# Performance work log

Measured on AMD Instinct MI355X. Metric: run time of the kernel, lower is better.

Reference implementation:

```python
import jax, jax.numpy as jnp
import numpy as np

N = 50000
E = 1600000
IN_C = 165
HID = 256
HEADS = 8
OUT_C = 2
NEG_SLOPE = 0.2


def setup_inputs() -> dict:
    key = jax.random.key(0)
    ks = jax.random.split(key, 10)
    x = jax.random.normal(ks[0], (N, IN_C), dtype=jnp.float32)
    edge_index = jax.random.randint(ks[1], (2, E), 0, N, dtype=jnp.int64)
    c1 = HID // HEADS  # 32 per-head channels in layer 1
    W1 = jax.random.normal(ks[2], (IN_C, HEADS * c1), dtype=jnp.float32) * (1.0 / np.sqrt(IN_C))
    att_src1 = jax.random.normal(ks[3], (HEADS, c1), dtype=jnp.float32) * 0.1
    att_dst1 = jax.random.normal(ks[4], (HEADS, c1), dtype=jnp.float32) * 0.1
    b1 = jnp.zeros((HEADS * c1,), dtype=jnp.float32)
    W2 = jax.random.normal(ks[5], (HID, 1 * OUT_C), dtype=jnp.float32) * (1.0 / np.sqrt(HID))
    att_src2 = jax.random.normal(ks[6], (1, OUT_C), dtype=jnp.float32) * 0.1
    att_dst2 = jax.random.normal(ks[7], (1, OUT_C), dtype=jnp.float32) * 0.1
    b2 = jnp.zeros((OUT_C,), dtype=jnp.float32)
    return {"x": x, "edge_index": edge_index, "W1": W1, "att_src1": att_src1,
            "att_dst1": att_dst1, "b1": b1, "W2": W2, "att_src2": att_src2,
            "att_dst2": att_dst2, "b2": b2}


def _gat_conv(x, src, dst, W, att_src, att_dst, bias, heads, concat):
    """PyG GATConv (eval mode, self-loops already appended to src/dst)."""
    n = x.shape[0]
    c = att_src.shape[1]
    h = (x @ W).reshape(n, heads, c)                      # [N, H, C]
    a_src = jnp.einsum('nhc,hc->nh', h, att_src)          # [N, H]
    a_dst = jnp.einsum('nhc,hc->nh', h, att_dst)
    e = a_src[src] + a_dst[dst]                           # [Et, H]
    e = jax.nn.leaky_relu(e, NEG_SLOPE)
    # segment softmax over incoming edges of each dst node
    e_max = jax.ops.segment_max(e, dst, num_segments=n)   # [N, H]
    e_exp = jnp.exp(e - e_max[dst])
    denom = jax.ops.segment_sum(e_exp, dst, num_segments=n)
    alpha = e_exp / denom[dst]                            # [Et, H]
    msg = alpha[:, :, None] * h[src]                      # [Et, H, C]
    out = jax.ops.segment_sum(msg, dst, num_segments=n)   # [N, H, C]
    if concat:
        out = out.reshape(n, heads * c)
    else:
        out = out.mean(axis=1)
    return out + bias


def reference(x, edge_index, W1, att_src1, att_dst1, b1, W2, att_src2, att_dst2, b2):
    n = x.shape[0]
    loops = jnp.arange(n, dtype=edge_index.dtype)
    src = jnp.concatenate([edge_index[0], loops])  # add_self_loops=True (PyG default)
    dst = jnp.concatenate([edge_index[1], loops])
    h = _gat_conv(x, src, dst, W1, att_src1, att_dst1, b1, HEADS, True)
    h = jax.nn.elu(h)
    out = _gat_conv(h, src, dst, W2, att_src2, att_dst2, b2, 1, False)
    return out
```

## Files before the change

### kernel.cpp

```cpp
#include <hip/hip_runtime.h>
#include <hip/hip_bf16.h>
#include <math.h>

#define N_NODES 50000
#define N_EDGES 1600000
#define ET (N_EDGES + N_NODES)
#define IN_C 165
#define HID 256
#define HEADS 8
#define C1 32
#define OUT_C 2
#define NEG_SLOPE 0.2f
#define TROWS 32
#define XSTR 36
#define GEMM_BLOCKS ((N_NODES + TROWS - 1) / TROWS)
#define SCB 2048
#define NPP ((N_NODES + 7) / 8)
#define CAPL 96

__device__ inline float lrelu(float v) { return v > 0.f ? v : NEG_SLOPE * v; }

__device__ inline unsigned short f32_bf16(float f) {
    unsigned u = __float_as_uint(f);
    return (unsigned short)((u + 0x7FFFu + ((u >> 16) & 1u)) >> 16);
}

__device__ __forceinline__ void gemm1_att_block(
        int row0, const float* __restrict__ x, const float* __restrict__ W,
        const float* __restrict__ att_src, const float* __restrict__ att_dst,
        unsigned short* __restrict__ h, float* __restrict__ a_src,
        float* __restrict__ a_dst, float* xs) {
    const int tid = threadIdx.x;
    const int nrow = (N_NODES - row0 < TROWS) ? (N_NODES - row0) : TROWS;
    const int lim = nrow * IN_C;
    for (int idx = tid; idx < TROWS * IN_C; idx += 256) {
        int r = idx / IN_C, k = idx - r * IN_C;
        xs[k * XSTR + r] = (idx < lim) ? x[(size_t)row0 * IN_C + idx] : 0.f;
    }
    __syncthreads();
    const int tr = tid >> 5;
    const int cq = tid & 31;
    const int c0 = cq * 8;
    float acc[4][8];
    #pragma unroll
    for (int j = 0; j < 4; ++j)
        #pragma unroll
        for (int q = 0; q < 8; ++q) acc[j][q] = 0.f;
    float4 xv = *(const float4*)(xs + tr * 4);
    float4 w0 = *(const float4*)(W + c0);
    float4 w1 = *(const float4*)(W + c0 + 4);
    #pragma unroll 3
    for (int k = 0; k < IN_C; ++k) {
        float4 xc = xv, a0 = w0, a1 = w1;
        if (k + 1 < IN_C) {
            xv = *(const float4*)(xs + (k + 1) * XSTR + tr * 4);
            w0 = *(const float4*)(W + (k + 1) * HID + c0);
            w1 = *(const float4*)(W + (k + 1) * HID + c0 + 4);
        }
        #pragma unroll
        for (int j = 0; j < 4; ++j) {
            float xj = (j == 0) ? xc.x : (j == 1) ? xc.y : (j == 2) ? xc.z : xc.w;
            acc[j][0] += xj * a0.x; acc[j][1] += xj * a0.y;
            acc[j][2] += xj * a0.z; acc[j][3] += xj * a0.w;
            acc[j][4] += xj * a1.x; acc[j][5] += xj * a1.y;
            acc[j][6] += xj * a1.z; acc[j][7] += xj * a1.w;
        }
    }
    #pragma unroll
    for (int j = 0; j < 4; ++j) {
        int gr = row0 + tr * 4 + j;
        if (gr < N_NODES) {
            unsigned p[4];
            #pragma unroll
            for (int q = 0; q < 4; ++q)
                p[q] = (unsigned)f32_bf16(acc[j][2*q]) |
                       ((unsigned)f32_bf16(acc[j][2*q+1]) << 16);
            *(uint4*)(h + (size_t)gr * HID + c0) = make_uint4(p[0], p[1], p[2], p[3]);
        }
    }
    {
        const int hd = cq >> 2;
        const float* as = att_src + hd * C1 + (cq & 3) * 8;
        const float* ad = att_dst + hd * C1 + (cq & 3) * 8;
        float av[8], dv[8];
        #pragma unroll
        for (int q = 0; q < 2; ++q) {
            float4 a4 = *(const float4*)(as + q * 4);
            float4 d4 = *(const float4*)(ad + q * 4);
            av[q*4+0]=a4.x; av[q*4+1]=a4.y; av[q*4+2]=a4.z; av[q*4+3]=a4.w;
            dv[q*4+0]=d4.x; dv[q*4+1]=d4.y; dv[q*4+2]=d4.z; dv[q*4+3]=d4.w;
        }
        float ps[4], pd[4];
        #pragma unroll
        for (int j = 0; j < 4; ++j) {
            float s = 0.f, d = 0.f;
            #pragma unroll
            for (int q = 0; q < 8; ++q) {
                s += acc[j][q] * av[q];
                d += acc[j][q] * dv[q];
            }
            ps[j] = s; pd[j] = d;
        }
        #pragma unroll
        for (int off = 1; off <= 2; off <<= 1) {
            #pragma unroll
            for (int j = 0; j < 4; ++j) {
                ps[j] += __shfl_xor(ps[j], off);
                pd[j] += __shfl_xor(pd[j], off);
            }
        }
        if ((cq & 3) == 0) {
            #pragma unroll
            for (int j = 0; j < 4; ++j) {
                int gr = row0 + tr * 4 + j;
                if (gr < N_NODES) {
                    a_src[gr * 8 + hd] = ps[j];
                    a_dst[gr * 8 + hd] = pd[j];
                }
            }
        }
    }
}

__global__ __launch_bounds__(256) void fusedAB_kernel(
        const float* __restrict__ x, const float* __restrict__ W,
        const float* __restrict__ att_src, const float* __restrict__ att_dst,
        unsigned short* __restrict__ h, float* __restrict__ a_src,
        float* __restrict__ a_dst,
        const int* __restrict__ src, const int* __restrict__ dst,
        int* __restrict__ deg, unsigned short* __restrict__ csr) {
    __shared__ float xs[IN_C * XSTR];
    if (blockIdx.x < GEMM_BLOCKS) {
        gemm1_att_block(blockIdx.x * TROWS, x, W, att_src, att_dst,
                        h, a_src, a_dst, xs);
    } else {
        const int sb  = blockIdx.x - GEMM_BLOCKS;
        const int cls = sb & 7;
        const int blk = sb >> 3;
        const int lo = cls * NPP;
        const int hi = (lo + NPP < N_NODES) ? lo + NPP : N_NODES;
        for (int e = blk * 256 + threadIdx.x; e < ET; e += (SCB >> 3) * 256) {
            int d = (e < N_EDGES) ? dst[e] : e - N_EDGES;
            if (d >= lo && d < hi) {
                int s = (e < N_EDGES) ? src[e] : d;
                int slot = atomicAdd(&deg[d], 1);
                csr[(size_t)d * CAPL + slot] = (unsigned short)s;
            }
        }
    }
}

__global__ __launch_bounds__(256) void agg1_fused_kernel(
        const int* __restrict__ deg, const unsigned short* __restrict__ csr,
        const float* __restrict__ a_src, const float* __restrict__ a_dst,
        const unsigned short* __restrict__ h1, const float* __restrict__ b1,
        const float* __restrict__ W2,
        const float* __restrict__ as2, const float* __restrict__ ad2,
        float4* __restrict__ pk, float* __restrict__ a2d) {
    int wid = (blockIdx.x * 256 + threadIdx.x) >> 6;
    int l = threadIdx.x & 63;
    if (wid >= N_NODES) return;
    const unsigned short* lst = csr + (size_t)wid * CAPL;
    const int n = deg[wid];
    const int hp = l >> 3;
    const float ad_p = a_dst[wid * 8 + hp];
    const int c = l * 4;
    float den = 0.f;
    float ax = 0.f, ay = 0.f, az = 0.f, aw = 0.f;
    int i = 0;
    for (; i + 8 <= n; i += 8) {
        int s[8];
        #pragma unroll
        for (int j = 0; j < 8; ++j) s[j] = lst[i + j];
        uint2 v[8];
        #pragma unroll
        for (int j = 0; j < 8; ++j)
            v[j] = *(const uint2*)(h1 + (size_t)s[j] * HID + c);
        float w[8];
        #pragma unroll
        for (int j = 0; j < 8; ++j)
            w[j] = __expf(lrelu(a_src[s[j] * 8 + hp] + ad_p));
        #pragma unroll
        for (int j = 0; j < 8; ++j) {
            den += w[j];
            ax += w[j] * __uint_as_float(v[j].x << 16);
            ay += w[j] * __uint_as_float(v[j].x & 0xFFFF0000u);
            az += w[j] * __uint_as_float(v[j].y << 16);
            aw += w[j] * __uint_as_float(v[j].y & 0xFFFF0000u);
        }
    }
    for (; i < n; ++i) {
        int s = lst[i];
        uint2 v = *(const uint2*)(h1 + (size_t)s * HID + c);
        float w = __expf(lrelu(a_src[s * 8 + hp] + ad_p));
        den += w;
        ax += w * __uint_as_float(v.x << 16);
        ay += w * __uint_as_float(v.x & 0xFFFF0000u);
        az += w * __uint_as_float(v.y << 16);
        aw += w * __uint_as_float(v.y & 0xFFFF0000u);
    }
    const float inv = 1.f / den;
    float4 bv = *(const float4*)(b1 + c);
    float o0 = ax * inv + bv.x, o1 = ay * inv + bv.y;
    float o2 = az * inv + bv.z, o3 = aw * inv + bv.w;
    o0 = o0 > 0.f ? o0 : expm1f(o0);
    o1 = o1 > 0.f ? o1 : expm1f(o1);
    o2 = o2 > 0.f ? o2 : expm1f(o2);
    o3 = o3 > 0.f ? o3 : expm1f(o3);
    const float* wv = W2 + l * 8;
    float4 w0 = *(const float4*)(wv);
    float4 w1 = *(const float4*)(wv + 4);
    float p0 = o0 * w0.x + o1 * w0.z + o2 * w1.x + o3 * w1.z;
    float p1 = o0 * w0.y + o1 * w0.w + o2 * w1.y + o3 * w1.w;
    #pragma unroll
    for (int off = 32; off; off >>= 1) {
        p0 += __shfl_down(p0, off);
        p1 += __shfl_down(p1, off);
    }
    if (l == 0) {
        pk[wid] = make_float4(p0, p1, p0 * as2[0] + p1 * as2[1], 0.f);
        a2d[wid] = p0 * ad2[0] + p1 * ad2[1];
    }
}

__global__ __launch_bounds__(256) void agg2_fused_kernel(
        const int* __restrict__ deg, const unsigned short* __restrict__ csr,
        const float4* __restrict__ pk, const float* __restrict__ a2d,
        const float* __restrict__ b2, float* __restrict__ out) {
    int t = blockIdx.x * 256 + threadIdx.x;
    int node = t >> 4;
    int l = t & 15;
    if (node >= N_NODES) return;
    const unsigned short* lst = csr + (size_t)node * CAPL;
    const int n = deg[node];
    const float adv = a2d[node];
    float sm = 0.f, acc0 = 0.f, acc1 = 0.f;
    for (int i = l; i < n; i += 16) {
        int s = lst[i];
        float4 pv = pk[s];
        float w = __expf(lrelu(pv.z + adv));
        sm += w;
        acc0 += w * pv.x;
        acc1 += w * pv.y;
    }
    #pragma unroll
    for (int off = 8; off; off >>= 1) {
        sm   += __shfl_xor(sm, off);
        acc0 += __shfl_xor(acc0, off);
        acc1 += __shfl_xor(acc1, off);
    }
    if (l == 0) {
        out[node * 2]     = acc0 / sm + b2[0];
        out[node * 2 + 1] = acc1 / sm + b2[1];
    }
}

extern "C" void kernel_launch(void* const* d_in, const int* in_sizes, int n_in,
                              void* d_out, int out_size, void* d_ws, size_t ws_size,
                              hipStream_t stream) {
    (void)in_sizes; (void)n_in; (void)out_size; (void)ws_size;
    const float* x        = (const float*)d_in[0];
    const int*   ei       = (const int*)d_in[1];
    const float* W1       = (const float*)d_in[2];
    const float* att_src1 = (const float*)d_in[3];
    const float* att_dst1 = (const float*)d_in[4];
    const float* b1       = (const float*)d_in[5];
    const float* W2       = (const float*)d_in[6];
    const float* att_src2 = (const float*)d_in[7];
    const float* att_dst2 = (const float*)d_in[8];
    const float* b2       = (const float*)d_in[9];
    float* out = (float*)d_out;

    const int* src = ei;
    const int* dst = ei + N_EDGES;

    char* ws = (char*)d_ws;
    size_t off = 0;
    unsigned short* h1 = (unsigned short*)(ws + off);
    off += (size_t)N_NODES * HID * 2;
    float* a_src1 = (float*)(ws + off); off += (size_t)N_NODES * HEADS * 4;
    float* a_dst1 = (float*)(ws + off); off += (size_t)N_NODES * HEADS * 4;
    float4* pk = (float4*)(ws + off); off += (size_t)N_NODES * 16;
    float* a2d = (float*)(ws + off); off += (size_t)N_NODES * 4;
    int* deg    = (int*)(ws + off); off += (size_t)N_NODES * 4;
    unsigned short* csr = (unsigned short*)(ws + off);
    off += (size_t)N_NODES * CAPL * 2;

    hipMemsetAsync(deg, 0, (size_t)N_NODES * 4, stream);

    const int NW = (N_NODES * 64 + 255) / 256;

    fusedAB_kernel<<<GEMM_BLOCKS + SCB, 256, 0, stream>>>(
        x, W1, att_src1, att_dst1, h1, a_src1, a_dst1, src, dst, deg, csr);

    agg1_fused_kernel<<<NW, 256, 0, stream>>>(
        deg, csr, a_src1, a_dst1, h1, b1, W2, att_src2, att_dst2, pk, a2d);

    agg2_fused_kernel<<<(N_NODES * 16 + 255) / 256, 256, 0, stream>>>(
        deg, csr, pk, a2d, b2, out);
}
```

Measured before the change: 350.6 us.

## Interleave GEMM/scatter blocks, vectorize edge scan, widen agg1 gathers to 16 bytes

The fused first kernel now interleaves GEMM and CSR-scatter blocks in groups so both kinds of work are spread across the launch. The scatter reads dst as int4 and handles self-loops in a separate pass. The layer-1 aggregation splits each wavefront into two halves that each take alternating edges and gather 16-byte bf16 vectors, then combines the halves with a cross-half shuffle. Layer 2 unrolls its edge loop by two and writes its output as float2. These changes aim to raise memory-level parallelism and cut instruction count in the gather-bound stages, at the cost of more registers and a more complex block-to-work mapping.

After: 345.7 us. Within noise of the previous version (-1.4%).

```diff
diff --git a/kernel.cpp b/kernel.cpp
--- a/kernel.cpp
+++ b/kernel.cpp
@@ -14,9 +14,12 @@
 #define TROWS 32
 #define XSTR 36
 #define GEMM_BLOCKS ((N_NODES + TROWS - 1) / TROWS)
-#define SCB 2048
 #define NPP ((N_NODES + 7) / 8)
 #define CAPL 96
+#define GGRP 196
+#define SGRP 256
+#define TGRP 452
+#define NE4 (N_EDGES / 4)
 
 __device__ inline float lrelu(float v) { return v > 0.f ? v : NEG_SLOPE * v; }
 
@@ -24,6 +27,9 @@
     unsigned u = __float_as_uint(f);
     return (unsigned short)((u + 0x7FFFu + ((u >> 16) & 1u)) >> 16);
 }
+
+__device__ inline float bflo(unsigned u) { return __uint_as_float(u << 16); }
+__device__ inline float bfhi(unsigned u) { return __uint_as_float(u & 0xFFFF0000u); }
 
 __device__ __forceinline__ void gemm1_att_block(
         int row0, const float* __restrict__ x, const float* __restrict__ W,
@@ -130,21 +136,42 @@
         const int* __restrict__ src, const int* __restrict__ dst,
         int* __restrict__ deg, unsigned short* __restrict__ csr) {
     __shared__ float xs[IN_C * XSTR];
-    if (blockIdx.x < GEMM_BLOCKS) {
-        gemm1_att_block(blockIdx.x * TROWS, x, W, att_src, att_dst,
-                        h, a_src, a_dst, xs);
+    const int g  = blockIdx.x >> 3;
+    const int xc = blockIdx.x & 7;
+    bool is_gemm;
+    int rank;
+    if (g < 448) {
+        const int hi4 = g >> 4, lo4 = g & 15;
+        if (lo4 < 7) { is_gemm = true;  rank = hi4 * 7 + lo4; }
+        else         { is_gemm = false; rank = hi4 * 9 + lo4 - 7; }
+    } else { is_gemm = false; rank = 252 + (g - 448); }
+
+    if (is_gemm) {
+        const int gid = rank * 8 + xc;
+        if (gid < GEMM_BLOCKS)
+            gemm1_att_block(gid * TROWS, x, W, att_src, att_dst,
+                            h, a_src, a_dst, xs);
     } else {
-        const int sb  = blockIdx.x - GEMM_BLOCKS;
-        const int cls = sb & 7;
-        const int blk = sb >> 3;
+        const int cls = xc;
+        const int blk = rank;
         const int lo = cls * NPP;
         const int hi = (lo + NPP < N_NODES) ? lo + NPP : N_NODES;
-        for (int e = blk * 256 + threadIdx.x; e < ET; e += (SCB >> 3) * 256) {
-            int d = (e < N_EDGES) ? dst[e] : e - N_EDGES;
-            if (d >= lo && d < hi) {
-                int s = (e < N_EDGES) ? src[e] : d;
-                int slot = atomicAdd(&deg[d], 1);
-                csr[(size_t)d * CAPL + slot] = (unsigned short)s;
+        const int t = blk * 256 + threadIdx.x;
+        if (t < hi - lo) {
+            int d = lo + t;
+            int slot = atomicAdd(&deg[d], 1);
+            csr[(size_t)d * CAPL + slot] = (unsigned short)d;
+        }
+        const int4* dst4 = (const int4*)dst;
+        for (int u = t; u < NE4; u += SGRP * 256) {
+            int4 dv = dst4[u];
+            #pragma unroll
+            for (int j = 0; j < 4; ++j) {
+                int d = (j == 0) ? dv.x : (j == 1) ? dv.y : (j == 2) ? dv.z : dv.w;
+                if (d >= lo && d < hi) {
+                    int slot = atomicAdd(&deg[d], 1);
+                    csr[(size_t)d * CAPL + slot] = (unsigned short)src[4 * u + j];
+                }
             }
         }
     }
@@ -153,69 +180,108 @@
 __global__ __launch_bounds__(256) void agg1_fused_kernel(
         const int* __restrict__ deg, const unsigned short* __restrict__ csr,
         const float* __restrict__ a_src, const float* __restrict__ a_dst,
-        const unsigned short* __restrict__ h1, const float* __restrict__ b1,
+        const unsigned short* __restrict__ h1, const float* __restrict__ bias1,
         const float* __restrict__ W2,
         const float* __restrict__ as2, const float* __restrict__ ad2,
         float4* __restrict__ pk, float* __restrict__ a2d) {
     int wid = (blockIdx.x * 256 + threadIdx.x) >> 6;
     int l = threadIdx.x & 63;
     if (wid >= N_NODES) return;
+    const int el = l >> 5;
+    const int q  = l & 31;
+    const int hd = q >> 2;
+    const int ch = q * 8;
     const unsigned short* lst = csr + (size_t)wid * CAPL;
     const int n = deg[wid];
-    const int hp = l >> 3;
-    const float ad_p = a_dst[wid * 8 + hp];
-    const int c = l * 4;
+    const float ad_p = a_dst[wid * 8 + hd];
     float den = 0.f;
-    float ax = 0.f, ay = 0.f, az = 0.f, aw = 0.f;
+    float acc[8];
+    #pragma unroll
+    for (int k = 0; k < 8; ++k) acc[k] = 0.f;
     int i = 0;
-    for (; i + 8 <= n; i += 8) {
+    for (; i + 16 <= n; i += 16) {
         int s[8];
         #pragma unroll
-        for (int j = 0; j < 8; ++j) s[j] = lst[i + j];
-        uint2 v[8];
+        for (int j = 0; j < 8; ++j) s[j] = lst[i + 2 * j + el];
+        uint4 v[8];
         #pragma unroll
         for (int j = 0; j < 8; ++j)
-            v[j] = *(const uint2*)(h1 + (size_t)s[j] * HID + c);
+            v[j] = *(const uint4*)(h1 + (size_t)s[j] * HID + ch);
         float w[8];
         #pragma unroll
         for (int j = 0; j < 8; ++j)
-            w[j] = __expf(lrelu(a_src[s[j] * 8 + hp] + ad_p));
+            w[j] = __expf(lrelu(a_src[s[j] * 8 + hd] + ad_p));
         #pragma unroll
         for (int j = 0; j < 8; ++j) {
             den += w[j];
-            ax += w[j] * __uint_as_float(v[j].x << 16);
-            ay += w[j] * __uint_as_float(v[j].x & 0xFFFF0000u);
-            az += w[j] * __uint_as_float(v[j].y << 16);
-            aw += w[j] * __uint_as_float(v[j].y & 0xFFFF0000u);
-        }
-    }
-    for (; i < n; ++i) {
-        int s = lst[i];
-        uint2 v = *(const uint2*)(h1 + (size_t)s * HID + c);
-        float w = __expf(lrelu(a_src[s * 8 + hp] + ad_p));
-        den += w;
-        ax += w * __uint_as_float(v.x << 16);
-        ay += w * __uint_as_float(v.x & 0xFFFF0000u);
-        az += w * __uint_as_float(v.y << 16);
-        aw += w * __uint_as_float(v.y & 0xFFFF0000u);
-    }
+            acc[0] += w[j] * bflo(v[j].x); acc[1] += w[j] * bfhi(v[j].x);
+            acc[2] += w[j] * bflo(v[j].y); acc[3] += w[j] * bfhi(v[j].y);
+            acc[4] += w[j] * bflo(v[j].z); acc[5] += w[j] * bfhi(v[j].z);
+            acc[6] += w[j] * bflo(v[j].w); acc[7] += w[j] * bfhi(v[j].w);
+        }
+    }
+    if (i + 8 <= n) {
+        int s[4];
+        #pragma unroll
+        for (int j = 0; j < 4; ++j) s[j] = lst[i + 2 * j + el];
+        uint4 v[4];
+        #pragma unroll
+        for (int j = 0; j < 4; ++j)
+            v[j] = *(const uint4*)(h1 + (size_t)s[j] * HID + ch);
+        float w[4];
+        #pragma unroll
+        for (int j = 0; j < 4; ++j)
+            w[j] = __expf(lrelu(a_src[s[j] * 8 + hd] + ad_p));
+        #pragma unroll
+        for (int j = 0; j < 4; ++j) {
+            den += w[j];
+            acc[0] += w[j] * bflo(v[j].x); acc[1] += w[j] * bfhi(v[j].x);
+            acc[2] += w[j] * bflo(v[j].y); acc[3] += w[j] * bfhi(v[j].y);
+            acc[4] += w[j] * bflo(v[j].z); acc[5] += w[j] * bfhi(v[j].z);
+            acc[6] += w[j] * bflo(v[j].w); acc[7] += w[j] * bfhi(v[j].w);
+        }
+        i += 8;
+    }
+    for (; i < n; i += 2) {
+        int e = i + el;
+        if (e < n) {
+            int s = lst[e];
+            uint4 v = *(const uint4*)(h1 + (size_t)s * HID + ch);
+            float w = __expf(lrelu(a_src[s * 8 + hd] + ad_p));
+            den += w;
+            acc[0] += w * bflo(v.x); acc[1] += w * bfhi(v.x);
+            acc[2] += w * bflo(v.y); acc[3] += w * bfhi(v.y);
+            acc[4] += w * bflo(v.z); acc[5] += w * bfhi(v.z);
+            acc[6] += w * bflo(v.w); acc[7] += w * bfhi(v.w);
+        }
+    }
+    den += __shfl_xor(den, 32);
+    #pragma unroll
+    for (int k = 0; k < 8; ++k) acc[k] += __shfl_xor(acc[k], 32);
+
     const float inv = 1.f / den;
-    float4 bv = *(const float4*)(b1 + c);
-    float o0 = ax * inv + bv.x, o1 = ay * inv + bv.y;
-    float o2 = az * inv + bv.z, o3 = aw * inv + bv.w;
-    o0 = o0 > 0.f ? o0 : expm1f(o0);
-    o1 = o1 > 0.f ? o1 : expm1f(o1);
-    o2 = o2 > 0.f ? o2 : expm1f(o2);
-    o3 = o3 > 0.f ? o3 : expm1f(o3);
-    const float* wv = W2 + l * 8;
+    float4 bva = *(const float4*)(bias1 + ch);
+    float4 bvb = *(const float4*)(bias1 + ch + 4);
+    float o[8];
+    o[0] = acc[0] * inv + bva.x; o[1] = acc[1] * inv + bva.y;
+    o[2] = acc[2] * inv + bva.z; o[3] = acc[3] * inv + bva.w;
+    o[4] = acc[4] * inv + bvb.x; o[5] = acc[5] * inv + bvb.y;
+    o[6] = acc[6] * inv + bvb.z; o[7] = acc[7] * inv + bvb.w;
+    #pragma unroll
+    for (int k = 0; k < 8; ++k) o[k] = o[k] > 0.f ? o[k] : expm1f(o[k]);
+    const float* wv = W2 + q * 16;
     float4 w0 = *(const float4*)(wv);
     float4 w1 = *(const float4*)(wv + 4);
-    float p0 = o0 * w0.x + o1 * w0.z + o2 * w1.x + o3 * w1.z;
-    float p1 = o0 * w0.y + o1 * w0.w + o2 * w1.y + o3 * w1.w;
-    #pragma unroll
-    for (int off = 32; off; off >>= 1) {
-        p0 += __shfl_down(p0, off);
-        p1 += __shfl_down(p1, off);
+    float4 w2 = *(const float4*)(wv + 8);
+    float4 w3 = *(const float4*)(wv + 12);
+    float p0 = o[0]*w0.x + o[1]*w0.z + o[2]*w1.x + o[3]*w1.z
+             + o[4]*w2.x + o[5]*w2.z + o[6]*w3.x + o[7]*w3.z;
+    float p1 = o[0]*w0.y + o[1]*w0.w + o[2]*w1.y + o[3]*w1.w
+             + o[4]*w2.y + o[5]*w2.w + o[6]*w3.y + o[7]*w3.w;
+    #pragma unroll
+    for (int off = 16; off; off >>= 1) {
+        p0 += __shfl_xor(p0, off);
+        p1 += __shfl_xor(p1, off);
     }
     if (l == 0) {
         pk[wid] = make_float4(p0, p1, p0 * as2[0] + p1 * as2[1], 0.f);
@@ -235,7 +301,17 @@
     const int n = deg[node];
     const float adv = a2d[node];
     float sm = 0.f, acc0 = 0.f, acc1 = 0.f;
-    for (int i = l; i < n; i += 16) {
+    int i = l;
+    for (; i + 16 < n; i += 32) {
+        int s0 = lst[i], s1 = lst[i + 16];
+        float4 p0 = pk[s0], p1 = pk[s1];
+        float w0 = __expf(lrelu(p0.z + adv));
+        float w1 = __expf(lrelu(p1.z + adv));
+        sm += w0 + w1;
+        acc0 += w0 * p0.x + w1 * p1.x;
+        acc1 += w0 * p0.y + w1 * p1.y;
+    }
+    for (; i < n; i += 16) {
         int s = lst[i];
         float4 pv = pk[s];
         float w = __expf(lrelu(pv.z + adv));
@@ -250,8 +326,8 @@
         acc1 += __shfl_xor(acc1, off);
     }
     if (l == 0) {
-        out[node * 2]     = acc0 / sm + b2[0];
-        out[node * 2 + 1] = acc1 / sm + b2[1];
+        *(float2*)(out + node * 2) =
+            make_float2(acc0 / sm + b2[0], acc1 / sm + b2[1]);
     }
 }
 
@@ -290,7 +366,7 @@
 
     const int NW = (N_NODES * 64 + 255) / 256;
 
-    fusedAB_kernel<<<GEMM_BLOCKS + SCB, 256, 0, stream>>>(
+    fusedAB_kernel<<<TGRP * 8, 256, 0, stream>>>(
         x, W1, att_src1, att_dst1, h1, a_src1, a_dst1, src, dst, deg, csr);
 
     agg1_fused_kernel<<<NW, 256, 0, stream>>>(
```
